# Optimization experiments

Hardware: AMD Instinct MI355X
Metric: run time of the kernel (lower is better)

Reference implementation:

```python
import jax, jax.numpy as jnp
import numpy as np
import math
from jax import lax

L = 16
T = 2 ** 14          # hash table size (power of 2 -> uint32 arithmetic is exact mod T)
F_DIM = 2
N_MIN, N_MAX = 16, 512
_B = math.exp((math.log(N_MAX) - math.log(N_MIN)) / (L - 1))
NS = [int(N_MIN * _B ** i) for i in range(L)]
PRIME = np.uint32(2654435761)


def setup_inputs() -> dict:
    key = jax.random.key(0)
    k1, k2 = jax.random.split(key)
    x = jax.random.uniform(k1, (8, 2, 512, 512), dtype=jnp.float32)
    hash_table = jax.random.uniform(k2, (L, T, F_DIM), dtype=jnp.float32) * 2e-4 - 1e-4
    return {"x": x, "hash_table": hash_table}


def reference(x, hash_table):
    b, c, h, w = x.shape
    feats = []
    for i, n in enumerate(NS):
        kh, kw = h // n, w // n
        # max_pool2d(x*n, (kh,kw), stride=1) -> [b, 2, h-kh+1, w-kw+1]
        g = lax.reduce_window(x * n, -jnp.inf, lax.max,
                              (1, 1, kh, kw), (1, 1, 1, 1), 'VALID')
        g = g.astype(jnp.uint32)  # trunc toward zero, values nonneg and small
        # prime-XOR hash; T is a power of two so uint32 wraparound matches int64 math mod T
        idx = (g[:, 0] ^ (g[:, 1] * PRIME)) % np.uint32(T)  # [b, gh, gw]
        f = hash_table[i][idx]                 # gather -> [b, gh, gw, F_DIM]
        f = jnp.transpose(f, (0, 3, 1, 2))     # [b, F_DIM, gh, gw]
        # bilinear upsample (half-pixel centers == align_corners=False)
        f = jax.image.resize(f, (b, F_DIM, h, w), method='bilinear')
        feats.append(f)
    return jnp.concatenate(feats, axis=1)       # [b, L*F_DIM, h, w]
```

## Files before the change

### kernel.cpp

```cpp
#include <hip/hip_runtime.h>
#include <stdint.h>

#define NLVL 16
#define TSIZE 16384
#define HW 512

__constant__ int c_n[NLVL] = {16,20,25,32,40,50,64,80,101,128,161,203,256,322,406,512};

__device__ __forceinline__ uint32_t pkmax(uint32_t a, uint32_t b) {
    uint32_t r;
    asm("v_pk_max_u16 %0, %1, %2" : "=v"(r) : "v"(a), "v"(b));
    return r;
}

template<int K>
__device__ __forceinline__ void do_tile(
        const int lvl, const int b, const int tx0, const int ty0,
        const float* __restrict__ x, const float* __restrict__ table,
        float* __restrict__ out, uint32_t* lds) {
    constexpr int gh = 513 - K;
    constexpr float s = (float)gh * (1.0f / 512.0f);
    const float nf = (float)c_n[lvl];
    const int tid = threadIdx.x;

    const float* xb0 = x + (size_t)b * 2 * HW * HW;
    const float* xb1 = xb0 + HW * HW;
    const float2* tb = (const float2*)table + (size_t)lvl * TSIZE;
    float* ob = out + ((size_t)b * 32 + lvl * 2) * HW * HW;

    if constexpr (K == 1) {
        const int btx = tid & 31, bty = tid >> 5;
        const int xo = tx0 + btx;
        for (int oy = bty; oy < 32; oy += 8) {
            const int y = ty0 + oy;
            const float v0 = xb0[y * HW + xo];
            const float v1 = xb1[y * HW + xo];
            const uint32_t g0 = (uint32_t)(v0 * nf);
            const uint32_t g1 = (uint32_t)(v1 * nf);
            const uint32_t idx = (g0 ^ (g1 * 2654435761u)) & (TSIZE - 1);
            const float2 f = tb[idx];
            const size_t o = (size_t)y * HW + xo;
            __builtin_nontemporal_store(f.x, &ob[o]);
            __builtin_nontemporal_store(f.y, &ob[o + (size_t)HW * HW]);
        }
        return;
    }

    uint32_t* S  = lds;
    uint32_t* V  = lds + 4096;
    uint32_t* Hm = lds;
    float4*   F4 = (float4*)(lds + 1200);

    const int gy_base = (int)floorf(((float)ty0 + 0.5f) * s - 0.5f);
    const int gx_base = (int)floorf(((float)tx0 + 0.5f) * s - 0.5f);
    const int rmin = max(gy_base, 0);
    const int cmin = max(gx_base, 0);
    const int nr = min(gy_base + 32, gh - 1) - rmin;
    const int nc = min(gx_base + 32, gh - 1) - cmin;
    const int Rr = nr + K;

    {
        const int wv = tid >> 6, c = tid & 63;
        const int xx = min(cmin + c, HW - 1);
        for (int r = wv; r < Rr; r += 4) {
            const int yy = rmin + r;
            const float v0 = xb0[yy * HW + xx];
            const float v1 = xb1[yy * HW + xx];
            S[r * 64 + c] = (uint32_t)(v0 * nf) | ((uint32_t)(v1 * nf) << 16);
        }
    }
    __syncthreads();

    {
        const int c = tid & 63, g = tid >> 6;
        const int R0 = 9 * g;
        const uint32_t* col = S + R0 * 64 + c;
        uint32_t e[K + 8];
#pragma unroll
        for (int t = 0; t < K + 8; ++t) e[t] = col[t * 64];
        uint32_t o[9];
        if constexpr (K >= 10) {
            uint32_t sfx[9];
            sfx[8] = e[8];
#pragma unroll
            for (int t = 7; t >= 0; --t) sfx[t] = pkmax(e[t], sfx[t + 1]);
            uint32_t run = e[9];
#pragma unroll
            for (int m = 9; m <= K + 7; ++m) {
                if (m > 9) run = pkmax(run, e[m]);
                if (m >= K - 1) o[m - K + 1] = pkmax(sfx[m - K + 1], run);
            }
        } else {
#pragma unroll
            for (int i = 0; i < 9; ++i) {
                uint32_t m = e[i];
#pragma unroll
                for (int t = 1; t < K; ++t) m = pkmax(m, e[i + t]);
                o[i] = m;
            }
        }
#pragma unroll
        for (int t = 0; t < 9; ++t) {
            const int i = R0 + t;
            if (i <= 32) V[i * 64 + c] = o[t];
        }
    }
    __syncthreads();

    if (tid < 132) {
        const int i = tid >> 2, g = tid & 3;
        if (g < 3) {
            constexpr int NE  = 12 + K - 1;
            constexpr int NCH = (NE + 3) >> 2;
            uint32_t f[NCH * 4];
            const uint4* rp = (const uint4*)(V + i * 64 + 12 * g);
#pragma unroll
            for (int cc = 0; cc < NCH; ++cc) {
                const uint4 q = rp[cc];
                f[4*cc] = q.x; f[4*cc+1] = q.y; f[4*cc+2] = q.z; f[4*cc+3] = q.w;
            }
            uint32_t wm[12];
            if constexpr (K >= 13) {
                uint32_t sfx[12];
                sfx[11] = f[11];
#pragma unroll
                for (int d = 10; d >= 0; --d) sfx[d] = pkmax(f[d], sfx[d + 1]);
                uint32_t run = f[12];
#pragma unroll
                for (int m = 12; m <= K + 10; ++m) {
                    if (m > 12) run = pkmax(run, f[m]);
                    if (m >= K - 1) wm[m - K + 1] = pkmax(sfx[m - K + 1], run);
                }
            } else {
#pragma unroll
                for (int d = 0; d < 12; ++d) {
                    uint32_t m = f[d];
#pragma unroll
                    for (int t = 1; t < K; ++t) m = pkmax(m, f[d + t]);
                    wm[d] = m;
                }
            }
            uint32_t* hw_ = Hm + i * 36 + 12 * g;
            ((uint4*)hw_)[0] = make_uint4(wm[0], wm[1], wm[2],  wm[3]);
            ((uint4*)hw_)[1] = make_uint4(wm[4], wm[5], wm[6],  wm[7]);
            ((uint4*)hw_)[2] = make_uint4(wm[8], wm[9], wm[10], wm[11]);
        }
    }
    __syncthreads();

    for (int p = tid; p < 33 * 34; p += 256) {
        const int i = p / 34, jj = p - i * 34;
        const uint32_t m = Hm[i * 36 + min(jj, nc)];
        const uint32_t idx = ((m & 0xFFFFu) ^ ((m >> 16) * 2654435761u)) & (TSIZE - 1);
        const float2 v = tb[idx];
        float2* Fp = (float2*)(F4 + i * 33);
        if (jj < 33) Fp[2 * jj] = v;
        if (jj >= 1) Fp[2 * jj - 1] = v;
    }
    __syncthreads();

    const int bty = tid >> 5, btx = tid & 31;
    const int xo = tx0 + btx;
    const float sxf = ((float)xo + 0.5f) * s - 0.5f;
    const float fxf = floorf(sxf);
    const float wx = sxf - fxf;
    const int x0i = (int)fxf;
    const int jx0 = min(max(x0i, 0), gh - 1) - cmin;
    const bool xclamp = (x0i < 0);
    for (int oy = bty; oy < 32; oy += 8) {
        const int y = ty0 + oy;
        const float syf = ((float)y + 0.5f) * s - 0.5f;
        const float fyf = floorf(syf);
        const float wy = syf - fyf;
        const int y0i = (int)fyf;
        const int iy0 = min(max(y0i, 0), gh - 1) - rmin;
        const int iy1 = min(max(y0i + 1, 0), gh - 1) - rmin;
        float4 a  = F4[iy0 * 33 + jx0];
        float4 bq = F4[iy1 * 33 + jx0];
        if (xclamp) { a.z = a.x; a.w = a.y; bq.z = bq.x; bq.w = bq.y; }
        const float w11 = wy * wx;
        const float w10 = wy - w11;
        const float w01 = wx - w11;
        const float w00 = 1.0f - wy - wx + w11;
        const float c0 = a.x * w00 + a.z * w01 + bq.x * w10 + bq.z * w11;
        const float c1 = a.y * w00 + a.w * w01 + bq.y * w10 + bq.w * w11;
        const size_t o = (size_t)y * HW + xo;
        __builtin_nontemporal_store(c0, &ob[o]);
        __builtin_nontemporal_store(c1, &ob[o + (size_t)HW * HW]);
    }
}

__global__ __launch_bounds__(256, 6) void fused_kernel(
        const float* __restrict__ x, const float* __restrict__ table,
        float* __restrict__ out) {
    __shared__ __align__(16) uint32_t lds[6272];

    const int bid  = blockIdx.x;
    const int b    = bid & 7;
    const int tile = (bid >> 3) & 255;
    const int lvl  = bid >> 11;
    const int tx0  = (tile & 15) * 32;
    const int ty0  = (tile >> 4) * 32;

    switch (lvl) {
        case  0: do_tile<32>( 0, b, tx0, ty0, x, table, out, lds); break;
        case  1: do_tile<25>( 1, b, tx0, ty0, x, table, out, lds); break;
        case  2: do_tile<20>( 2, b, tx0, ty0, x, table, out, lds); break;
        case  3: do_tile<16>( 3, b, tx0, ty0, x, table, out, lds); break;
        case  4: do_tile<12>( 4, b, tx0, ty0, x, table, out, lds); break;
        case  5: do_tile<10>( 5, b, tx0, ty0, x, table, out, lds); break;
        case  6: do_tile< 8>( 6, b, tx0, ty0, x, table, out, lds); break;
        case  7: do_tile< 6>( 7, b, tx0, ty0, x, table, out, lds); break;
        case  8: do_tile< 5>( 8, b, tx0, ty0, x, table, out, lds); break;
        case  9: do_tile< 4>( 9, b, tx0, ty0, x, table, out, lds); break;
        case 10: do_tile< 3>(10, b, tx0, ty0, x, table, out, lds); break;
        case 11: do_tile< 2>(11, b, tx0, ty0, x, table, out, lds); break;
        case 12: do_tile< 2>(12, b, tx0, ty0, x, table, out, lds); break;
        case 13: do_tile< 1>(13, b, tx0, ty0, x, table, out, lds); break;
        case 14: do_tile< 1>(14, b, tx0, ty0, x, table, out, lds); break;
        default: do_tile< 1>(15, b, tx0, ty0, x, table, out, lds); break;
    }
}

extern "C" void kernel_launch(void* const* d_in, const int* in_sizes, int n_in,
                              void* d_out, int out_size, void* d_ws, size_t ws_size,
                              hipStream_t stream) {
    const float* x     = (const float*)d_in[0];
    const float* table = (const float*)d_in[1];
    float* out         = (float*)d_out;
    (void)d_ws; (void)ws_size;

    fused_kernel<<<dim3(NLVL * 256 * 8), dim3(256), 0, stream>>>(x, table, out);
}
```

Baseline: 124.2 us.

## Fuse vertical max pass with global loads and hash gather into horizontal pass

The vertical max-pool pass now reads x straight from global memory into registers, with each wave covering 8 rows, instead of staging the full input column block in LDS first. The hash gather is folded into the horizontal-max threads, which write float2 features directly, and the interpolation stage reads four float2 values instead of duplicated float4 pairs. This removes two barriers and the S staging buffer and shrinks LDS use. In exchange the vertical pass issues overlapping redundant global loads across waves, only 99 threads run the hash gather, and the launch-bounds occupancy hint is dropped.

Result: faster. 110.2 us (-11.3%).

```diff
diff --git a/kernel.cpp b/kernel.cpp
--- a/kernel.cpp
+++ b/kernel.cpp
@@ -33,10 +33,8 @@
         const int xo = tx0 + btx;
         for (int oy = bty; oy < 32; oy += 8) {
             const int y = ty0 + oy;
-            const float v0 = xb0[y * HW + xo];
-            const float v1 = xb1[y * HW + xo];
-            const uint32_t g0 = (uint32_t)(v0 * nf);
-            const uint32_t g1 = (uint32_t)(v1 * nf);
+            const uint32_t g0 = (uint32_t)(xb0[y * HW + xo] * nf);
+            const uint32_t g1 = (uint32_t)(xb1[y * HW + xo] * nf);
             const uint32_t idx = (g0 ^ (g1 * 2654435761u)) & (TSIZE - 1);
             const float2 f = tb[idx];
             const size_t o = (size_t)y * HW + xo;
@@ -46,38 +44,27 @@
         return;
     }
 
-    uint32_t* S  = lds;
-    uint32_t* V  = lds + 4096;
-    uint32_t* Hm = lds;
-    float4*   F4 = (float4*)(lds + 1200);
+    uint32_t* V   = lds;
+    float2*  feat = (float2*)(lds + 33 * 68);
 
     const int gy_base = (int)floorf(((float)ty0 + 0.5f) * s - 0.5f);
     const int gx_base = (int)floorf(((float)tx0 + 0.5f) * s - 0.5f);
     const int rmin = max(gy_base, 0);
     const int cmin = max(gx_base, 0);
-    const int nr = min(gy_base + 32, gh - 1) - rmin;
-    const int nc = min(gx_base + 32, gh - 1) - cmin;
-    const int Rr = nr + K;
 
     {
         const int wv = tid >> 6, c = tid & 63;
+        const int r0 = 8 * wv;
         const int xx = min(cmin + c, HW - 1);
-        for (int r = wv; r < Rr; r += 4) {
-            const int yy = rmin + r;
+        const int ybase = rmin + r0;
+        uint32_t e[K + 8];
+#pragma unroll
+        for (int t = 0; t < K + 8; ++t) {
+            const int yy = min(ybase + t, HW - 1);
             const float v0 = xb0[yy * HW + xx];
             const float v1 = xb1[yy * HW + xx];
-            S[r * 64 + c] = (uint32_t)(v0 * nf) | ((uint32_t)(v1 * nf) << 16);
-        }
-    }
-    __syncthreads();
-
-    {
-        const int c = tid & 63, g = tid >> 6;
-        const int R0 = 9 * g;
-        const uint32_t* col = S + R0 * 64 + c;
-        uint32_t e[K + 8];
-#pragma unroll
-        for (int t = 0; t < K + 8; ++t) e[t] = col[t * 64];
+            e[t] = (uint32_t)(v0 * nf) | ((uint32_t)(v1 * nf) << 16);
+        }
         uint32_t o[9];
         if constexpr (K >= 10) {
             uint32_t sfx[9];
@@ -100,62 +87,51 @@
             }
         }
 #pragma unroll
-        for (int t = 0; t < 9; ++t) {
-            const int i = R0 + t;
-            if (i <= 32) V[i * 64 + c] = o[t];
-        }
+        for (int t = 0; t < 9; ++t) V[(r0 + t) * 68 + c] = o[t];
     }
     __syncthreads();
 
-    if (tid < 132) {
-        const int i = tid >> 2, g = tid & 3;
-        if (g < 3) {
-            constexpr int NE  = 12 + K - 1;
-            constexpr int NCH = (NE + 3) >> 2;
-            uint32_t f[NCH * 4];
-            const uint4* rp = (const uint4*)(V + i * 64 + 12 * g);
-#pragma unroll
-            for (int cc = 0; cc < NCH; ++cc) {
-                const uint4 q = rp[cc];
-                f[4*cc] = q.x; f[4*cc+1] = q.y; f[4*cc+2] = q.z; f[4*cc+3] = q.w;
-            }
-            uint32_t wm[12];
-            if constexpr (K >= 13) {
-                uint32_t sfx[12];
-                sfx[11] = f[11];
-#pragma unroll
-                for (int d = 10; d >= 0; --d) sfx[d] = pkmax(f[d], sfx[d + 1]);
-                uint32_t run = f[12];
-#pragma unroll
-                for (int m = 12; m <= K + 10; ++m) {
-                    if (m > 12) run = pkmax(run, f[m]);
-                    if (m >= K - 1) wm[m - K + 1] = pkmax(sfx[m - K + 1], run);
-                }
-            } else {
-#pragma unroll
-                for (int d = 0; d < 12; ++d) {
-                    uint32_t m = f[d];
-#pragma unroll
-                    for (int t = 1; t < K; ++t) m = pkmax(m, f[d + t]);
-                    wm[d] = m;
-                }
-            }
-            uint32_t* hw_ = Hm + i * 36 + 12 * g;
-            ((uint4*)hw_)[0] = make_uint4(wm[0], wm[1], wm[2],  wm[3]);
-            ((uint4*)hw_)[1] = make_uint4(wm[4], wm[5], wm[6],  wm[7]);
-            ((uint4*)hw_)[2] = make_uint4(wm[8], wm[9], wm[10], wm[11]);
-        }
-    }
-    __syncthreads();
-
-    for (int p = tid; p < 33 * 34; p += 256) {
-        const int i = p / 34, jj = p - i * 34;
-        const uint32_t m = Hm[i * 36 + min(jj, nc)];
-        const uint32_t idx = ((m & 0xFFFFu) ^ ((m >> 16) * 2654435761u)) & (TSIZE - 1);
-        const float2 v = tb[idx];
-        float2* Fp = (float2*)(F4 + i * 33);
-        if (jj < 33) Fp[2 * jj] = v;
-        if (jj >= 1) Fp[2 * jj - 1] = v;
+    if (tid < 99) {
+        const int i = tid / 3, g = tid % 3;
+        constexpr int NE  = 12 + K - 1;
+        constexpr int NCH = (NE + 3) >> 2;
+        uint32_t f[NCH * 4];
+        const uint4* rp = (const uint4*)(V + i * 68 + 12 * g);
+#pragma unroll
+        for (int cc = 0; cc < NCH; ++cc) {
+            const uint4 q = rp[cc];
+            f[4*cc] = q.x; f[4*cc+1] = q.y; f[4*cc+2] = q.z; f[4*cc+3] = q.w;
+        }
+        uint32_t wm[12];
+        if constexpr (K >= 13) {
+            uint32_t sfx[12];
+            sfx[11] = f[11];
+#pragma unroll
+            for (int d = 10; d >= 0; --d) sfx[d] = pkmax(f[d], sfx[d + 1]);
+            uint32_t run = f[12];
+#pragma unroll
+            for (int m = 12; m <= K + 10; ++m) {
+                if (m > 12) run = pkmax(run, f[m]);
+                if (m >= K - 1) wm[m - K + 1] = pkmax(sfx[m - K + 1], run);
+            }
+        } else {
+#pragma unroll
+            for (int d = 0; d < 12; ++d) {
+                uint32_t m = f[d];
+#pragma unroll
+                for (int t = 1; t < K; ++t) m = pkmax(m, f[d + t]);
+                wm[d] = m;
+            }
+        }
+#pragma unroll
+        for (int d = 0; d < 12; ++d) {
+            const int j = 12 * g + d;
+            if (j < 33) {
+                const uint32_t m = wm[d];
+                const uint32_t idx = ((m & 0xFFFFu) ^ ((m >> 16) * 2654435761u)) & (TSIZE - 1);
+                feat[i * 34 + j] = tb[idx];
+            }
+        }
     }
     __syncthreads();
 
@@ -166,7 +142,7 @@
     const float wx = sxf - fxf;
     const int x0i = (int)fxf;
     const int jx0 = min(max(x0i, 0), gh - 1) - cmin;
-    const bool xclamp = (x0i < 0);
+    const int jx1 = min(max(x0i + 1, 0), gh - 1) - cmin;
     for (int oy = bty; oy < 32; oy += 8) {
         const int y = ty0 + oy;
         const float syf = ((float)y + 0.5f) * s - 0.5f;
@@ -175,25 +151,24 @@
         const int y0i = (int)fyf;
         const int iy0 = min(max(y0i, 0), gh - 1) - rmin;
         const int iy1 = min(max(y0i + 1, 0), gh - 1) - rmin;
-        float4 a  = F4[iy0 * 33 + jx0];
-        float4 bq = F4[iy1 * 33 + jx0];
-        if (xclamp) { a.z = a.x; a.w = a.y; bq.z = bq.x; bq.w = bq.y; }
+        const float2 f00 = feat[iy0 * 34 + jx0], f01 = feat[iy0 * 34 + jx1];
+        const float2 f10 = feat[iy1 * 34 + jx0], f11 = feat[iy1 * 34 + jx1];
         const float w11 = wy * wx;
         const float w10 = wy - w11;
         const float w01 = wx - w11;
         const float w00 = 1.0f - wy - wx + w11;
-        const float c0 = a.x * w00 + a.z * w01 + bq.x * w10 + bq.z * w11;
-        const float c1 = a.y * w00 + a.w * w01 + bq.y * w10 + bq.w * w11;
+        const float c0 = f00.x * w00 + f01.x * w01 + f10.x * w10 + f11.x * w11;
+        const float c1 = f00.y * w00 + f01.y * w01 + f10.y * w10 + f11.y * w11;
         const size_t o = (size_t)y * HW + xo;
         __builtin_nontemporal_store(c0, &ob[o]);
         __builtin_nontemporal_store(c1, &ob[o + (size_t)HW * HW]);
     }
 }
 
-__global__ __launch_bounds__(256, 6) void fused_kernel(
+__global__ __launch_bounds__(256) void fused_kernel(
         const float* __restrict__ x, const float* __restrict__ table,
         float* __restrict__ out) {
-    __shared__ __align__(16) uint32_t lds[6272];
+    __shared__ __align__(16) uint32_t lds[33 * 68 + 33 * 34 * 2];
 
     const int bid  = blockIdx.x;
     const int b    = bid & 7;
```
